# Performance work log

Measured on AMD Instinct MI355X. Metric: run time of the kernel, lower is better.

The kernel has to match this reference:

```python
import jax, jax.numpy as jnp
import numpy as np

# ---- config (matches init_kwargs) ----
ORIGIN_OCC_SHAPE = (16, 200, 200)   # (D_oi, H_oi, W_oi)
INPUT_SIZE = (900, 1600)            # (ih, iw)
DOWN_SAMPLE = 8
GRID_CONFIG = {
    'x_bound': [-40.0, 40.0, 0.4],
    'y_bound': [-40.0, 40.0, 0.4],
    'z_bound': [-1.0, 5.4, 0.4],
    'd_bound': [2.0, 58.0, 1.0],
}


def setup_inputs() -> dict:
    key = jax.random.key(0)
    occ_feature = jax.random.normal(key, (1, 32, 16, 200, 200), dtype=jnp.float32)
    # realistic nuScenes-like intrinsics
    K = jnp.array([[[1266.4, 0.0, 816.3],
                    [0.0, 1266.4, 491.5],
                    [0.0, 0.0, 1.0]]], dtype=jnp.float32)
    # cam->ego: camera looks along ego +x; cam z -> ego x, cam x -> ego -y, cam y -> ego -z
    T = jnp.array([[[0.0, 0.0, 1.0, 1.5],
                    [-1.0, 0.0, 0.0, 0.0],
                    [0.0, -1.0, 0.0, 1.5],
                    [0.0, 0.0, 0.0, 1.0]]], dtype=jnp.float32)
    return {'occ_feature': occ_feature, 'K': K, 'T': T}


def get_sampling_points():
    ih, iw = INPUT_SIZE
    fh, fw = ih // DOWN_SAMPLE, iw // DOWN_SAMPLE
    d0, d1, dstep = GRID_CONFIG['d_bound']
    fd = int((d1 - d0) // dstep)
    x = jnp.linspace(0.0, iw - 1.0, fw)
    y = jnp.linspace(0.0, ih - 1.0, fh)
    d = jnp.linspace(d0, d1, fd)
    gd, gy, gx = jnp.meshgrid(d, y, x, indexing='ij')   # (fd, fh, fw)
    # homogeneous image points scaled by depth: [x*d, y*d, d, 1]
    pts = jnp.stack([gx * gd, gy * gd, gd, jnp.ones_like(gd)], axis=-1)
    return pts  # (fd, fh, fw, 4)


def grid_sample_3d(vol, grid):
    """Trilinear grid_sample, padding_mode='zeros', align_corners=True.
    vol: (B,C,D,H,W); grid: (B,Do,Ho,Wo,3) with (x,y,z) in [-1,1] -> (W,H,D)."""
    B, C, D, H, W = vol.shape
    gx, gy, gz = grid[..., 0], grid[..., 1], grid[..., 2]
    x = (gx + 1.0) * 0.5 * (W - 1)
    y = (gy + 1.0) * 0.5 * (H - 1)
    z = (gz + 1.0) * 0.5 * (D - 1)
    x0 = jnp.floor(x); y0 = jnp.floor(y); z0 = jnp.floor(z)
    tx = x - x0; ty = y - y0; tz = z - z0
    vol_flat = vol.reshape(B, C, D * H * W)

    def corner(zc, yc, xc, w):
        valid = (xc >= 0) & (xc <= W - 1) & (yc >= 0) & (yc <= H - 1) & (zc >= 0) & (zc <= D - 1)
        zi = jnp.clip(zc, 0, D - 1).astype(jnp.int32)
        yi = jnp.clip(yc, 0, H - 1).astype(jnp.int32)
        xi = jnp.clip(xc, 0, W - 1).astype(jnp.int32)
        idx = ((zi * H + yi) * W + xi).reshape(B, 1, -1)          # (B,1,M)
        g = jnp.take_along_axis(vol_flat, idx, axis=2)            # (B,C,M)
        wm = jnp.where(valid, w, 0.0).reshape(B, 1, -1)
        return g * wm

    out = (corner(z0, y0, x0, (1 - tz) * (1 - ty) * (1 - tx))
           + corner(z0, y0, x0 + 1, (1 - tz) * (1 - ty) * tx)
           + corner(z0, y0 + 1, x0, (1 - tz) * ty * (1 - tx))
           + corner(z0, y0 + 1, x0 + 1, (1 - tz) * ty * tx)
           + corner(z0 + 1, y0, x0, tz * (1 - ty) * (1 - tx))
           + corner(z0 + 1, y0, x0 + 1, tz * (1 - ty) * tx)
           + corner(z0 + 1, y0 + 1, x0, tz * ty * (1 - tx))
           + corner(z0 + 1, y0 + 1, x0 + 1, tz * ty * tx))
    Do, Ho, Wo = grid.shape[1:4]
    return out.reshape(B, C, Do, Ho, Wo)


def volume_transform(occ_feature, K, T):
    B, C, D_occ, H_occ, W_occ = occ_feature.shape
    D_oi, H_oi, W_oi = ORIGIN_OCC_SHAPE
    ratio = (W_oi / W_occ, H_oi / H_occ, D_oi / D_occ)
    xb, yb, zb = GRID_CONFIG['x_bound'], GRID_CONFIG['y_bound'], GRID_CONFIG['z_bound']

    # ego -> ego-feature-grid affine (4x4)
    e2f = jnp.eye(4, dtype=jnp.float32)
    e2f = e2f.at[0, 0].set(1.0 / xb[2] / ratio[0])
    e2f = e2f.at[1, 1].set(1.0 / yb[2] / ratio[1])
    e2f = e2f.at[2, 2].set(1.0 / zb[2] / ratio[2])
    e2f = e2f.at[0, 3].set(-xb[0] / xb[2] / ratio[0])
    e2f = e2f.at[1, 3].set(-yb[0] / yb[2] / ratio[1])
    e2f = e2f.at[2, 3].set(-zb[0] / zb[2] / ratio[2])

    # cam2img 4x4 with K in top-left, then invert (matches torch.inverse path)
    cam2img = jnp.tile(jnp.eye(4, dtype=K.dtype)[None], (B, 1, 1))
    cam2img = cam2img.at[:, :3, :3].set(K)
    img2cam = jnp.linalg.inv(cam2img)                  # (B,4,4)

    # fused projection matrix: ego2egofeat @ T @ img2cam
    M = jnp.einsum('ij,bjk,bkl->bil', e2f, T, img2cam)  # (B,4,4)

    pts = get_sampling_points()                         # (fd,fh,fw,4)
    feat_pts = jnp.einsum('bij,dhwj->bdhwi', M, pts)[..., :3]  # (B,fd,fh,fw,3)

    norm = jnp.array([W_occ - 1, H_occ - 1, D_occ - 1], dtype=jnp.float32)
    grid = feat_pts / norm * 2.0 - 1.0

    sampled = grid_sample_3d(occ_feature, grid)         # (B,C,fd,fh,fw)
    return jnp.sum(sampled, axis=2)                     # (B,C,fh,fw)


def reference(occ_feature, K, T):
    return volume_transform(occ_feature, K, T)
```

## Files before the change

### kernel.cpp

```cpp
#include <hip/hip_runtime.h>

#define FD 56
#define FH 112
#define FW 200
#define VD 16
#define VH 200
#define VW 200
#define NC 32
#define NPIX (FH * FW)
#define NS   (VD * VH * VW)
#define CSTRIDE NS

typedef float f2v __attribute__((ext_vector_type(2)));
typedef f2v uf2v4 __attribute__((aligned(4)));
typedef _Float16 h4 __attribute__((ext_vector_type(4)));
typedef h4 uh4 __attribute__((aligned(8)));
typedef _Float16 h8 __attribute__((ext_vector_type(8)));

__device__ inline void compute_M(const float* Km, const float* Tm, float* M) {
    float a = Km[0], b = Km[1], c = Km[2];
    float d = Km[3], e = Km[4], f = Km[5];
    float g = Km[6], h = Km[7], i = Km[8];
    float A00 = e * i - f * h, A01 = c * h - b * i, A02 = b * f - c * e;
    float A10 = f * g - d * i, A11 = a * i - c * g, A12 = c * d - a * f;
    float A20 = d * h - e * g, A21 = b * g - a * h, A22 = a * e - b * d;
    float det = a * A00 + b * A10 + c * A20;
    float r = 1.0f / det;
    float Ki[9] = {A00 * r, A01 * r, A02 * r,
                   A10 * r, A11 * r, A12 * r,
                   A20 * r, A21 * r, A22 * r};
    float R[4][4];
    for (int rr = 0; rr < 4; ++rr) {
        for (int cc = 0; cc < 3; ++cc)
            R[rr][cc] = Tm[rr * 4 + 0] * Ki[0 * 3 + cc]
                      + Tm[rr * 4 + 1] * Ki[1 * 3 + cc]
                      + Tm[rr * 4 + 2] * Ki[2 * 3 + cc];
        R[rr][3] = Tm[rr * 4 + 3];
    }
    const float s[3] = {2.5f, 2.5f, 2.5f};
    const float t[3] = {100.0f, 100.0f, 2.5f};
    for (int rr = 0; rr < 3; ++rr)
        for (int cc = 0; cc < 4; ++cc)
            M[rr * 4 + cc] = s[rr] * R[rr][cc] + t[rr] * R[3][cc];
}

__global__ __launch_bounds__(256)
void vt_transpose_h(const float* __restrict__ vol, _Float16* __restrict__ volT,
                    const float* __restrict__ Km, const float* __restrict__ Tm) {
    __shared__ float tile[256 * 33];
    __shared__ int s_skip;
    const int t  = threadIdx.x;
    const int s0 = blockIdx.x * 256;

    if (t == 0) {
        float M[12];
        compute_M(Km, Tm, M);
        const float b00 = M[0], b01 = M[1], b02 = M[2],  tx3 = M[3];
        const float b10 = M[4], b11 = M[5], b12 = M[6],  ty3 = M[7];
        const float b20 = M[8], b21 = M[9], b22 = M[10], tz3 = M[11];
        const float C00 = b11 * b22 - b12 * b21;
        const float C01 = b02 * b21 - b01 * b22;
        const float C02 = b01 * b12 - b02 * b11;
        const float C10 = b12 * b20 - b10 * b22;
        const float C11 = b00 * b22 - b02 * b20;
        const float C12 = b02 * b10 - b00 * b12;
        const float C20 = b10 * b21 - b11 * b20;
        const float C21 = b01 * b20 - b00 * b21;
        const float C22 = b00 * b11 - b01 * b10;
        const float det = b00 * C00 + b01 * C10 + b02 * C20;
        int skip = 0;
        if (fabsf(det) > 1e-12f) {
            const float r = 1.0f / det;
            const float ix0 = C00 * r, ix1 = C01 * r, ix2 = C02 * r;
            const float iy0 = C10 * r, iy1 = C11 * r, iy2 = C12 * r;
            const float iz0 = C20 * r, iz1 = C21 * r, iz2 = C22 * r;
            const float cx = -(ix0 * tx3 + ix1 * ty3 + ix2 * tz3);
            const float cy = -(iy0 * tx3 + iy1 * ty3 + iy2 * tz3);
            const float cz = -(iz0 * tx3 + iz1 * ty3 + iz2 * tz3);
            const int send = s0 + 255;
            const int z0 = s0 / (VH * VW), z1 = send / (VH * VW);
            float ylo = 0.0f, yhi = (float)(VH - 1);
            if (z0 == z1) {
                const int r0 = s0 - z0 * (VH * VW);
                ylo = (float)(r0 / VW);
                yhi = (float)((r0 + 255) / VW);
            }
            const float EXP = 1.25f;
            const float lo[3] = {0.0f - EXP, ylo - EXP, (float)z0 - EXP};
            const float hi[3] = {(float)(VW - 1) + EXP, yhi + EXP, (float)z1 + EXP};
            const float SLK = 10.0f;
            const float gc[6][3] = {
                { iz0,  iz1,  iz2},
                {-iz0, -iz1, -iz2},
                { ix0,  ix1,  ix2},
                {1599.f*iz0 - ix0, 1599.f*iz1 - ix1, 1599.f*iz2 - ix2},
                { iy0,  iy1,  iy2},
                { 899.f*iz0 - iy0,  899.f*iz1 - iy1,  899.f*iz2 - iy2},
            };
            const float gd0[6] = {cz - 2.0f + 0.1f, 58.0f + 0.1f - cz,
                                  cx + SLK, 1599.f * cz - cx + SLK,
                                  cy + SLK,  899.f * cz - cy + SLK};
            for (int q = 0; q < 6; ++q) {
                float m = gd0[q];
                for (int j = 0; j < 3; ++j)
                    m += (gc[q][j] > 0.0f) ? gc[q][j] * hi[j] : gc[q][j] * lo[j];
                if (m < 0.0f) { skip = 1; break; }
            }
        }
        s_skip = skip;
    }
    __syncthreads();
    if (s_skip) return;

#pragma unroll
    for (int c = 0; c < NC; ++c)
        tile[t * 33 + c] = __builtin_nontemporal_load(vol + (size_t)c * CSTRIDE + s0 + t);
    __syncthreads();
    const int rs  = t >> 2;
    const int ch8 = (t & 3) * 8;
#pragma unroll
    for (int j = 0; j < 4; ++j) {
        const int sl = j * 64 + rs;
        const float* r = &tile[sl * 33 + ch8];
        h8 pk = {(_Float16)r[0], (_Float16)r[1], (_Float16)r[2], (_Float16)r[3],
                 (_Float16)r[4], (_Float16)r[5], (_Float16)r[6], (_Float16)r[7]};
        *(h8*)(volT + (size_t)(s0 + sl) * NC + ch8) = pk;
    }
}

__global__ __launch_bounds__(256)
void vt_sample_th(const _Float16* __restrict__ volT,
                  const float* __restrict__ Km,
                  const float* __restrict__ Tm,
                  float* __restrict__ out) {
    __shared__ float sM[12];
    if (threadIdx.x == 0) compute_M(Km, Tm, sM);
    __syncthreads();

    const int t    = threadIdx.x;
    const int wv   = t >> 6;
    const int lane = t & 63;
    const int chq  = lane & 7;
    const int pixl = lane >> 3;
    const int c0   = chq * 4;
    const int p    = blockIdx.x * 32 + wv * 8 + pixl;
    const int py   = p / FW;
    const int px   = p - py * FW;

    const float gx = (float)px * (1599.0f / 199.0f);
    const float gy = (float)py * (899.0f / 111.0f);

    const float m03 = sM[3], m13 = sM[7], m23 = sM[11];
    const float ax = sM[0] * gx + sM[1] * gy + sM[2];
    const float ay = sM[4] * gx + sM[5] * gy + sM[6];
    const float az = sM[8] * gx + sM[9] * gy + sM[10];

    float dlo = 2.0f, dhi = 58.0f;
    {
        const float A[3]  = {ax, ay, az};
        const float Bv[3] = {m03, m13, m23};
        const float HI[3] = {(float)VW, (float)VH, (float)VD};
        for (int q = 0; q < 3; ++q) {
            float a = A[q], b = Bv[q], hi = HI[q];
            if (a > 0.0f)      { dlo = fmaxf(dlo, (-1.0f - b) / a); dhi = fminf(dhi, (hi - b) / a); }
            else if (a < 0.0f) { dlo = fmaxf(dlo, (hi - b) / a);    dhi = fminf(dhi, (-1.0f - b) / a); }
            else if (!(b > -1.0f && b < hi)) { dlo = 1e30f; dhi = -1e30f; }
        }
    }
    int klo = (int)ceilf((dlo - 2.0f) * (55.0f / 56.0f));
    int khi = (int)floorf((dhi - 2.0f) * (55.0f / 56.0f));
    klo = max(klo - 1, 0);
    khi = min(khi + 1, FD - 1);

    float acc0 = 0.0f, acc1 = 0.0f, acc2 = 0.0f, acc3 = 0.0f;

#pragma unroll 2
    for (int k = klo; k <= khi; ++k) {
        const float gd = 2.0f + (float)k * (56.0f / 55.0f);
        const float fx = fmaf(ax, gd, m03);
        const float fy = fmaf(ay, gd, m13);
        const float fz = fmaf(az, gd, m23);

        const bool valid = (fx > -1.0f) && (fx < (float)VW) &&
                           (fy > -1.0f) && (fy < (float)VH) &&
                           (fz > -1.0f) && (fz < (float)VD);
        const float vm = valid ? 1.0f : 0.0f;

        const float xf = floorf(fx), yf = floorf(fy), zf = floorf(fz);
        const float tx = fx - xf, ty = fy - yf, tz = fz - zf;
        const int ix = (int)xf, iy = (int)yf, iz = (int)zf;

        const float wx0 = (ix >= 0)     ? (1.0f - tx) : 0.0f;
        const float wx1 = (ix < VW - 1) ? tx          : 0.0f;
        const float wy0 = (iy >= 0)     ? (1.0f - ty) : 0.0f;
        const float wy1 = (iy < VH - 1) ? ty          : 0.0f;
        const float wz0 = ((iz >= 0)     ? (1.0f - tz) : 0.0f) * vm;
        const float wz1 = ((iz < VD - 1) ? tz          : 0.0f) * vm;

        const int xi0 = min(max(ix,     0), VW - 1);
        const int xi1 = min(max(ix + 1, 0), VW - 1);
        const int yo0 = min(max(iy,     0), VH - 1) * VW;
        const int yo1 = min(max(iy + 1, 0), VH - 1) * VW;
        const int zo0 = min(max(iz,     0), VD - 1) * (VH * VW);
        const int zo1 = min(max(iz + 1, 0), VD - 1) * (VH * VW);

        const int o000 = ((zo0 + yo0 + xi0) << 5) + c0;
        const int o001 = ((zo0 + yo0 + xi1) << 5) + c0;
        const int o010 = ((zo0 + yo1 + xi0) << 5) + c0;
        const int o011 = ((zo0 + yo1 + xi1) << 5) + c0;
        const int o100 = ((zo1 + yo0 + xi0) << 5) + c0;
        const int o101 = ((zo1 + yo0 + xi1) << 5) + c0;
        const int o110 = ((zo1 + yo1 + xi0) << 5) + c0;
        const int o111 = ((zo1 + yo1 + xi1) << 5) + c0;

        const h4 v000 = *(const uh4*)(volT + o000);
        const h4 v001 = *(const uh4*)(volT + o001);
        const h4 v010 = *(const uh4*)(volT + o010);
        const h4 v011 = *(const uh4*)(volT + o011);
        const h4 v100 = *(const uh4*)(volT + o100);
        const h4 v101 = *(const uh4*)(volT + o101);
        const h4 v110 = *(const uh4*)(volT + o110);
        const h4 v111 = *(const uh4*)(volT + o111);

        const float w000 = wz0 * wy0 * wx0, w001 = wz0 * wy0 * wx1;
        const float w010 = wz0 * wy1 * wx0, w011 = wz0 * wy1 * wx1;
        const float w100 = wz1 * wy0 * wx0, w101 = wz1 * wy0 * wx1;
        const float w110 = wz1 * wy1 * wx0, w111 = wz1 * wy1 * wx1;

        acc0 += w000 * (float)v000.x + w001 * (float)v001.x
              + w010 * (float)v010.x + w011 * (float)v011.x
              + w100 * (float)v100.x + w101 * (float)v101.x
              + w110 * (float)v110.x + w111 * (float)v111.x;
        acc1 += w000 * (float)v000.y + w001 * (float)v001.y
              + w010 * (float)v010.y + w011 * (float)v011.y
              + w100 * (float)v100.y + w101 * (float)v101.y
              + w110 * (float)v110.y + w111 * (float)v111.y;
        acc2 += w000 * (float)v000.z + w001 * (float)v001.z
              + w010 * (float)v010.z + w011 * (float)v011.z
              + w100 * (float)v100.z + w101 * (float)v101.z
              + w110 * (float)v110.z + w111 * (float)v111.z;
        acc3 += w000 * (float)v000.w + w001 * (float)v001.w
              + w010 * (float)v010.w + w011 * (float)v011.w
              + w100 * (float)v100.w + w101 * (float)v101.w
              + w110 * (float)v110.w + w111 * (float)v111.w;
    }

    out[(size_t)(c0 + 0) * NPIX + p] = acc0;
    out[(size_t)(c0 + 1) * NPIX + p] = acc1;
    out[(size_t)(c0 + 2) * NPIX + p] = acc2;
    out[(size_t)(c0 + 3) * NPIX + p] = acc3;
}

__global__ __launch_bounds__(256)
void vt_sample_direct(const float* __restrict__ vol,
                      const float* __restrict__ Km,
                      const float* __restrict__ Tm,
                      float* __restrict__ out) {
    __shared__ float sM[12];
    if (threadIdx.x == 0) compute_M(Km, Tm, sM);
    __syncthreads();

    const int cg   = blockIdx.x & 3;
    const int pg   = blockIdx.x >> 2;
    const int lane = threadIdx.x & 63;
    const int wv   = threadIdx.x >> 6;
    const int c0   = (cg * 4 + wv) * 2;
    const int p    = pg * 64 + lane;
    const int py   = p / FW;
    const int px   = p - py * FW;

    const float gx = (float)px * (1599.0f / 199.0f);
    const float gy = (float)py * (899.0f / 111.0f);

    const float m03 = sM[3], m13 = sM[7], m23 = sM[11];
    const float ax = sM[0] * gx + sM[1] * gy + sM[2];
    const float ay = sM[4] * gx + sM[5] * gy + sM[6];
    const float az = sM[8] * gx + sM[9] * gy + sM[10];

    float dlo = 2.0f, dhi = 58.0f;
    {
        const float A[3]  = {ax, ay, az};
        const float Bv[3] = {m03, m13, m23};
        const float HI[3] = {(float)VW, (float)VH, (float)VD};
        for (int q = 0; q < 3; ++q) {
            float a = A[q], b = Bv[q], hi = HI[q];
            if (a > 0.0f)      { dlo = fmaxf(dlo, (-1.0f - b) / a); dhi = fminf(dhi, (hi - b) / a); }
            else if (a < 0.0f) { dlo = fmaxf(dlo, (hi - b) / a);    dhi = fminf(dhi, (-1.0f - b) / a); }
            else if (!(b > -1.0f && b < hi)) { dlo = 1e30f; dhi = -1e30f; }
        }
    }
    int klo = (int)ceilf((dlo - 2.0f) * (55.0f / 56.0f));
    int khi = (int)floorf((dhi - 2.0f) * (55.0f / 56.0f));
    klo = max(klo - 1, 0);
    khi = min(khi + 1, FD - 1);

    const float* __restrict__ volc0 = vol + (size_t)c0 * CSTRIDE;
    const float* __restrict__ volc1 = volc0 + CSTRIDE;
    float acc0 = 0.0f, acc1 = 0.0f;

#pragma unroll 2
    for (int k = klo; k <= khi; ++k) {
        const float gd = 2.0f + (float)k * (56.0f / 55.0f);
        const float fx = fmaf(ax, gd, m03);
        const float fy = fmaf(ay, gd, m13);
        const float fz = fmaf(az, gd, m23);

        const bool valid = (fx > -1.0f) && (fx < (float)VW) &&
                           (fy > -1.0f) && (fy < (float)VH) &&
                           (fz > -1.0f) && (fz < (float)VD);
        const float vm = valid ? 1.0f : 0.0f;

        const float xf = floorf(fx), yf = floorf(fy), zf = floorf(fz);
        const float tx = fx - xf, ty = fy - yf, tz = fz - zf;
        const int ix = (int)xf, iy = (int)yf, iz = (int)zf;

        float wlo = (ix >= 0) ? (1.0f - tx) : tx;
        wlo = (ix >= VW - 1) ? 0.0f : wlo;
        float whi = (ix >= 0) ? tx : 0.0f;
        whi = (ix >= VW - 1) ? (1.0f - tx) : whi;

        const float wy0 = (iy >= 0)     ? (1.0f - ty) : 0.0f;
        const float wy1 = (iy < VH - 1) ? ty          : 0.0f;
        const float wz0 = ((iz >= 0)     ? (1.0f - tz) : 0.0f) * vm;
        const float wz1 = ((iz < VD - 1) ? tz          : 0.0f) * vm;
        const float w00 = wz0 * wy0, w01 = wz0 * wy1;
        const float w10 = wz1 * wy0, w11 = wz1 * wy1;

        const int xi0 = min(max(ix, 0), VW - 2);
        const int yo0 = min(max(iy,     0), VH - 1) * VW;
        const int yo1 = min(max(iy + 1, 0), VH - 1) * VW;
        const int zo0 = min(max(iz,     0), VD - 1) * (VH * VW);
        const int zo1 = min(max(iz + 1, 0), VD - 1) * (VH * VW);

        const int o00 = zo0 + yo0 + xi0, o01 = zo0 + yo1 + xi0;
        const int o10 = zo1 + yo0 + xi0, o11 = zo1 + yo1 + xi0;

        const f2v a00 = *(const uf2v4*)(volc0 + o00);
        const f2v a01 = *(const uf2v4*)(volc0 + o01);
        const f2v a10 = *(const uf2v4*)(volc0 + o10);
        const f2v a11 = *(const uf2v4*)(volc0 + o11);
        const f2v b00 = *(const uf2v4*)(volc1 + o00);
        const f2v b01 = *(const uf2v4*)(volc1 + o01);
        const f2v b10 = *(const uf2v4*)(volc1 + o10);
        const f2v b11 = *(const uf2v4*)(volc1 + o11);

        acc0 += w00 * (wlo * a00.x + whi * a00.y) + w01 * (wlo * a01.x + whi * a01.y)
              + w10 * (wlo * a10.x + whi * a10.y) + w11 * (wlo * a11.x + whi * a11.y);
        acc1 += w00 * (wlo * b00.x + whi * b00.y) + w01 * (wlo * b01.x + whi * b01.y)
              + w10 * (wlo * b10.x + whi * b10.y) + w11 * (wlo * b11.x + whi * b11.y);
    }

    out[c0 * NPIX + p]       = acc0;
    out[(c0 + 1) * NPIX + p] = acc1;
}

extern "C" void kernel_launch(void* const* d_in, const int* in_sizes, int n_in,
                              void* d_out, int out_size, void* d_ws, size_t ws_size,
                              hipStream_t stream) {
    (void)in_sizes; (void)n_in; (void)out_size;
    const float* vol = (const float*)d_in[0];
    const float* Km  = (const float*)d_in[1];
    const float* Tm  = (const float*)d_in[2];
    float* out = (float*)d_out;

    const size_t need = (size_t)NS * NC * sizeof(_Float16);
    if (ws_size >= need) {
        _Float16* volT = (_Float16*)d_ws;
        vt_transpose_h<<<dim3(NS / 256), dim3(256), 0, stream>>>(vol, volT, Km, Tm);
        vt_sample_th<<<dim3(NPIX / 32), dim3(256), 0, stream>>>(volT, Km, Tm, out);
    } else {
        vt_sample_direct<<<dim3(1400), dim3(256), 0, stream>>>(vol, Km, Tm, out);
    }
}
```

Baseline: 145.5 us.

## Compact transposed fp16 volume to frustum bounding box and remap blocks per XCD

Adds a one-block setup kernel that computes the projection matrix and a voxel bounding box covering every sampling ray across all depths, and stores both in a small header in the workspace. The transpose kernel now skips blocks outside that box and writes the fp16 channel-last copy into a compact box-sized buffer. The sampling kernel clamps indices to the box and reads from the compact layout, which keeps the working set smaller and more cache-friendly. It also remaps block indices so each XCD handles a contiguous pixel range. The cost is an extra kernel launch, per-voxel index arithmetic in the transpose, and reliance on the box bound being conservative enough to keep results correct.

```diff
diff --git a/kernel.cpp b/kernel.cpp
--- a/kernel.cpp
+++ b/kernel.cpp
@@ -44,73 +44,143 @@
             M[rr * 4 + cc] = s[rr] * R[rr][cc] + t[rr] * R[3][cc];
 }
 
+__global__ __launch_bounds__(64)
+void vt_setup(const float* __restrict__ Km, const float* __restrict__ Tm,
+              float* __restrict__ hdr) {
+    __shared__ float sM[12];
+    const int t = threadIdx.x;
+    if (t == 0) compute_M(Km, Tm, sM);
+    __syncthreads();
+    float m[12];
+#pragma unroll
+    for (int i = 0; i < 12; ++i) m[i] = sM[i];
+
+    int bx0 = 0x7fffffff, by0 = 0x7fffffff, bz0 = 0x7fffffff;
+    int bx1 = -1, by1 = -1, bz1 = -1;
+    if (t < FD) {
+        const float gd = 2.0f + (float)t * (56.0f / 55.0f);
+        const float HIq[3] = {(float)VW, (float)VH, (float)VD};
+        float lo[3], hi[3];
+        bool ok = true;
+#pragma unroll
+        for (int q = 0; q < 3; ++q) {
+            const float axx  = m[q * 4 + 0] * gd * 1599.0f;
+            const float byy  = m[q * 4 + 1] * gd * 899.0f;
+            const float base = m[q * 4 + 2] * gd + m[q * 4 + 3];
+            lo[q] = base + fminf(axx, 0.0f) + fminf(byy, 0.0f);
+            hi[q] = base + fmaxf(axx, 0.0f) + fmaxf(byy, 0.0f);
+            if (!(lo[q] < HIq[q] && hi[q] > -1.0f)) ok = false;
+        }
+        if (ok) {
+            const int dmax[3] = {VW - 1, VH - 1, VD - 1};
+#pragma unroll
+            for (int q = 0; q < 3; ++q) {
+                int i0 = (int)floorf(fmaxf(lo[q], -2.0f)) - 1;
+                int i1 = (int)floorf(fminf(hi[q], HIq[q] + 1.0f)) + 2;
+                i0 = max(i0, 0);
+                i1 = min(i1, dmax[q]);
+                if (q == 0) { bx0 = i0; bx1 = i1; }
+                else if (q == 1) { by0 = i0; by1 = i1; }
+                else { bz0 = i0; bz1 = i1; }
+            }
+        }
+    }
+#pragma unroll
+    for (int s = 1; s < 64; s <<= 1) {
+        bx0 = min(bx0, __shfl_xor(bx0, s));
+        bx1 = max(bx1, __shfl_xor(bx1, s));
+        by0 = min(by0, __shfl_xor(by0, s));
+        by1 = max(by1, __shfl_xor(by1, s));
+        bz0 = min(bz0, __shfl_xor(bz0, s));
+        bz1 = max(bz1, __shfl_xor(bz1, s));
+    }
+    if (t == 0) {
+        if (bx1 < bx0 || by1 < by0 || bz1 < bz0) {
+            bx0 = by0 = bz0 = 0; bx1 = by1 = bz1 = 0;
+        }
+#pragma unroll
+        for (int i = 0; i < 12; ++i) hdr[i] = m[i];
+        int* hi = (int*)hdr;
+        hi[12] = bx0; hi[13] = by0; hi[14] = bz0;
+        hi[15] = bx1 - bx0 + 1;
+        hi[16] = by1 - by0 + 1;
+        hi[17] = bz1 - bz0 + 1;
+    }
+}
+
 __global__ __launch_bounds__(256)
-void vt_transpose_h(const float* __restrict__ vol, _Float16* __restrict__ volT,
-                    const float* __restrict__ Km, const float* __restrict__ Tm) {
+void vt_transpose_h(const float* __restrict__ vol, const float* __restrict__ hdr,
+                    _Float16* __restrict__ volT) {
     __shared__ float tile[256 * 33];
-    __shared__ int s_skip;
+    __shared__ int sh[8];
     const int t  = threadIdx.x;
     const int s0 = blockIdx.x * 256;
 
     if (t == 0) {
-        float M[12];
-        compute_M(Km, Tm, M);
-        const float b00 = M[0], b01 = M[1], b02 = M[2],  tx3 = M[3];
-        const float b10 = M[4], b11 = M[5], b12 = M[6],  ty3 = M[7];
-        const float b20 = M[8], b21 = M[9], b22 = M[10], tz3 = M[11];
-        const float C00 = b11 * b22 - b12 * b21;
-        const float C01 = b02 * b21 - b01 * b22;
-        const float C02 = b01 * b12 - b02 * b11;
-        const float C10 = b12 * b20 - b10 * b22;
-        const float C11 = b00 * b22 - b02 * b20;
-        const float C12 = b02 * b10 - b00 * b12;
-        const float C20 = b10 * b21 - b11 * b20;
-        const float C21 = b01 * b20 - b00 * b21;
-        const float C22 = b00 * b11 - b01 * b10;
-        const float det = b00 * C00 + b01 * C10 + b02 * C20;
+        const int* hint = (const int*)hdr;
+        const int cx0 = hint[12], cy0 = hint[13], cz0 = hint[14];
+        const int cw = hint[15], chh = hint[16], cd = hint[17];
+        const int send = s0 + 255;
+        const int z0 = s0 / (VH * VW), z1 = send / (VH * VW);
+        int ry0 = 0, ry1 = VH - 1;
+        if (z0 == z1) {
+            const int r0 = s0 - z0 * (VH * VW);
+            ry0 = r0 / VW;
+            ry1 = (r0 + 255) / VW;
+        }
         int skip = 0;
-        if (fabsf(det) > 1e-12f) {
-            const float r = 1.0f / det;
-            const float ix0 = C00 * r, ix1 = C01 * r, ix2 = C02 * r;
-            const float iy0 = C10 * r, iy1 = C11 * r, iy2 = C12 * r;
-            const float iz0 = C20 * r, iz1 = C21 * r, iz2 = C22 * r;
-            const float cx = -(ix0 * tx3 + ix1 * ty3 + ix2 * tz3);
-            const float cy = -(iy0 * tx3 + iy1 * ty3 + iy2 * tz3);
-            const float cz = -(iz0 * tx3 + iz1 * ty3 + iz2 * tz3);
-            const int send = s0 + 255;
-            const int z0 = s0 / (VH * VW), z1 = send / (VH * VW);
-            float ylo = 0.0f, yhi = (float)(VH - 1);
-            if (z0 == z1) {
-                const int r0 = s0 - z0 * (VH * VW);
-                ylo = (float)(r0 / VW);
-                yhi = (float)((r0 + 255) / VW);
+        if (z1 < cz0 || z0 > cz0 + cd - 1) skip = 1;
+        if (ry1 < cy0 || ry0 > cy0 + chh - 1) skip = 1;
+        if (!skip) {
+            const float b00 = hdr[0], b01 = hdr[1], b02 = hdr[2],  tx3 = hdr[3];
+            const float b10 = hdr[4], b11 = hdr[5], b12 = hdr[6],  ty3 = hdr[7];
+            const float b20 = hdr[8], b21 = hdr[9], b22 = hdr[10], tz3 = hdr[11];
+            const float C00 = b11 * b22 - b12 * b21;
+            const float C01 = b02 * b21 - b01 * b22;
+            const float C02 = b01 * b12 - b02 * b11;
+            const float C10 = b12 * b20 - b10 * b22;
+            const float C11 = b00 * b22 - b02 * b20;
+            const float C12 = b02 * b10 - b00 * b12;
+            const float C20 = b10 * b21 - b11 * b20;
+            const float C21 = b01 * b20 - b00 * b21;
+            const float C22 = b00 * b11 - b01 * b10;
+            const float det = b00 * C00 + b01 * C10 + b02 * C20;
+            if (fabsf(det) > 1e-12f) {
+                const float r = 1.0f / det;
+                const float ix0 = C00 * r, ix1 = C01 * r, ix2 = C02 * r;
+                const float iy0 = C10 * r, iy1 = C11 * r, iy2 = C12 * r;
+                const float iz0 = C20 * r, iz1 = C21 * r, iz2 = C22 * r;
+                const float cx = -(ix0 * tx3 + ix1 * ty3 + ix2 * tz3);
+                const float cy = -(iy0 * tx3 + iy1 * ty3 + iy2 * tz3);
+                const float cz = -(iz0 * tx3 + iz1 * ty3 + iz2 * tz3);
+                const float EXP = 1.25f;
+                const float lo[3] = {0.0f - EXP, (float)ry0 - EXP, (float)z0 - EXP};
+                const float hi[3] = {(float)(VW - 1) + EXP, (float)ry1 + EXP, (float)z1 + EXP};
+                const float SLK = 10.0f;
+                const float gc[6][3] = {
+                    { iz0,  iz1,  iz2},
+                    {-iz0, -iz1, -iz2},
+                    { ix0,  ix1,  ix2},
+                    {1599.f*iz0 - ix0, 1599.f*iz1 - ix1, 1599.f*iz2 - ix2},
+                    { iy0,  iy1,  iy2},
+                    { 899.f*iz0 - iy0,  899.f*iz1 - iy1,  899.f*iz2 - iy2},
+                };
+                const float gd0[6] = {cz - 2.0f + 0.1f, 58.0f + 0.1f - cz,
+                                      cx + SLK, 1599.f * cz - cx + SLK,
+                                      cy + SLK,  899.f * cz - cy + SLK};
+                for (int q = 0; q < 6; ++q) {
+                    float mx = gd0[q];
+                    for (int j = 0; j < 3; ++j)
+                        mx += (gc[q][j] > 0.0f) ? gc[q][j] * hi[j] : gc[q][j] * lo[j];
+                    if (mx < 0.0f) { skip = 1; break; }
+                }
             }
-            const float EXP = 1.25f;
-            const float lo[3] = {0.0f - EXP, ylo - EXP, (float)z0 - EXP};
-            const float hi[3] = {(float)(VW - 1) + EXP, yhi + EXP, (float)z1 + EXP};
-            const float SLK = 10.0f;
-            const float gc[6][3] = {
-                { iz0,  iz1,  iz2},
-                {-iz0, -iz1, -iz2},
-                { ix0,  ix1,  ix2},
-                {1599.f*iz0 - ix0, 1599.f*iz1 - ix1, 1599.f*iz2 - ix2},
-                { iy0,  iy1,  iy2},
-                { 899.f*iz0 - iy0,  899.f*iz1 - iy1,  899.f*iz2 - iy2},
-            };
-            const float gd0[6] = {cz - 2.0f + 0.1f, 58.0f + 0.1f - cz,
-                                  cx + SLK, 1599.f * cz - cx + SLK,
-                                  cy + SLK,  899.f * cz - cy + SLK};
-            for (int q = 0; q < 6; ++q) {
-                float m = gd0[q];
-                for (int j = 0; j < 3; ++j)
-                    m += (gc[q][j] > 0.0f) ? gc[q][j] * hi[j] : gc[q][j] * lo[j];
-                if (m < 0.0f) { skip = 1; break; }
-            }
-        }
-        s_skip = skip;
+        }
+        sh[0] = skip; sh[1] = cx0; sh[2] = cy0; sh[3] = cz0;
+        sh[4] = cw; sh[5] = chh; sh[6] = cd; sh[7] = chh * cw;
     }
     __syncthreads();
-    if (s_skip) return;
+    if (sh[0]) return;
 
 #pragma unroll
     for (int c = 0; c < NC; ++c)
@@ -118,23 +188,41 @@
     __syncthreads();
     const int rs  = t >> 2;
     const int ch8 = (t & 3) * 8;
+    const int cx0 = sh[1], cy0 = sh[2], cz0 = sh[3];
+    const int cw = sh[4], chh = sh[5], cd = sh[6], chw = sh[7];
 #pragma unroll
     for (int j = 0; j < 4; ++j) {
         const int sl = j * 64 + rs;
+        const int s  = s0 + sl;
+        const int z   = s / (VH * VW);
+        const int rem = s - z * (VH * VW);
+        const int y   = rem / VW;
+        const int x   = rem - y * VW;
+        const int ex = x - cx0, ey = y - cy0, ez = z - cz0;
+        if (ex < 0 || ex >= cw || ey < 0 || ey >= chh || ez < 0 || ez >= cd) continue;
         const float* r = &tile[sl * 33 + ch8];
         h8 pk = {(_Float16)r[0], (_Float16)r[1], (_Float16)r[2], (_Float16)r[3],
                  (_Float16)r[4], (_Float16)r[5], (_Float16)r[6], (_Float16)r[7]};
-        *(h8*)(volT + (size_t)(s0 + sl) * NC + ch8) = pk;
+        *(h8*)(volT + ((size_t)(ez * chw + ey * cw + ex) << 5) + ch8) = pk;
     }
 }
 
 __global__ __launch_bounds__(256)
 void vt_sample_th(const _Float16* __restrict__ volT,
-                  const float* __restrict__ Km,
-                  const float* __restrict__ Tm,
+                  const float* __restrict__ hdr,
                   float* __restrict__ out) {
     __shared__ float sM[12];
-    if (threadIdx.x == 0) compute_M(Km, Tm, sM);
+    __shared__ int sc[8];
+    if (threadIdx.x < 12) sM[threadIdx.x] = hdr[threadIdx.x];
+    if (threadIdx.x == 0) {
+        const int* hint = (const int*)hdr;
+        const int x0 = hint[12], y0 = hint[13], z0 = hint[14];
+        const int cw = hint[15], chh = hint[16], cd = hint[17];
+        sc[0] = x0; sc[1] = x0 + cw - 1;
+        sc[2] = y0; sc[3] = y0 + chh - 1;
+        sc[4] = z0; sc[5] = z0 + cd - 1;
+        sc[6] = cw; sc[7] = chh * cw;
+    }
     __syncthreads();
 
     const int t    = threadIdx.x;
@@ -143,7 +231,14 @@
     const int chq  = lane & 7;
     const int pixl = lane >> 3;
     const int c0   = chq * 4;
-    const int p    = blockIdx.x * 32 + wv * 8 + pixl;
+
+    const int nwg = NPIX / 32;
+    const int qc  = nwg >> 3, rc = nwg & 7;
+    const int xcd = (int)blockIdx.x & 7;
+    const int idx = (int)blockIdx.x >> 3;
+    const int sb  = (xcd < rc ? xcd * (qc + 1) : rc * (qc + 1) + (xcd - rc) * qc) + idx;
+
+    const int p    = sb * 32 + wv * 8 + pixl;
     const int py   = p / FW;
     const int px   = p - py * FW;
 
@@ -154,6 +249,9 @@
     const float ax = sM[0] * gx + sM[1] * gy + sM[2];
     const float ay = sM[4] * gx + sM[5] * gy + sM[6];
     const float az = sM[8] * gx + sM[9] * gy + sM[10];
+
+    const int X0 = sc[0], X1 = sc[1], Y0 = sc[2], Y1 = sc[3];
+    const int Z0 = sc[4], Z1 = sc[5], CWr = sc[6], CHWr = sc[7];
 
     float dlo = 2.0f, dhi = 58.0f;
     {
@@ -197,12 +295,12 @@
         const float wz0 = ((iz >= 0)     ? (1.0f - tz) : 0.0f) * vm;
         const float wz1 = ((iz < VD - 1) ? tz          : 0.0f) * vm;
 
-        const int xi0 = min(max(ix,     0), VW - 1);
-        const int xi1 = min(max(ix + 1, 0), VW - 1);
-        const int yo0 = min(max(iy,     0), VH - 1) * VW;
-        const int yo1 = min(max(iy + 1, 0), VH - 1) * VW;
-        const int zo0 = min(max(iz,     0), VD - 1) * (VH * VW);
-        const int zo1 = min(max(iz + 1, 0), VD - 1) * (VH * VW);
+        const int xi0 = min(max(ix,     X0), X1) - X0;
+        const int xi1 = min(max(ix + 1, X0), X1) - X0;
+        const int yo0 = (min(max(iy,     Y0), Y1) - Y0) * CWr;
+        const int yo1 = (min(max(iy + 1, Y0), Y1) - Y0) * CWr;
+        const int zo0 = (min(max(iz,     Z0), Z1) - Z0) * CHWr;
+        const int zo1 = (min(max(iz + 1, Z0), Z1) - Z0) * CHWr;
 
         const int o000 = ((zo0 + yo0 + xi0) << 5) + c0;
         const int o001 = ((zo0 + yo0 + xi1) << 5) + c0;
@@ -241,8 +339,8 @@
               + w110 * (float)v110.z + w111 * (float)v111.z;
         acc3 += w000 * (float)v000.w + w001 * (float)v001.w
               + w010 * (float)v010.w + w011 * (float)v011.w
-              + w100 * (float)v100.w + w101 * (float)v101.w
-              + w110 * (float)v110.w + w111 * (float)v111.w;
+              + w110 * (float)v110.w + w111 * (float)v111.w
+              + w100 * (float)v100.w + w101 * (float)v101.w;
     }
 
     out[(size_t)(c0 + 0) * NPIX + p] = acc0;
@@ -363,11 +461,13 @@
     const float* Tm  = (const float*)d_in[2];
     float* out = (float*)d_out;
 
-    const size_t need = (size_t)NS * NC * sizeof(_Float16);
+    const size_t need = 256 + (size_t)NS * NC * sizeof(_Float16);
     if (ws_size >= need) {
-        _Float16* volT = (_Float16*)d_ws;
-        vt_transpose_h<<<dim3(NS / 256), dim3(256), 0, stream>>>(vol, volT, Km, Tm);
-        vt_sample_th<<<dim3(NPIX / 32), dim3(256), 0, stream>>>(volT, Km, Tm, out);
+        float* hdr = (float*)d_ws;
+        _Float16* volT = (_Float16*)((char*)d_ws + 256);
+        vt_setup<<<dim3(1), dim3(64), 0, stream>>>(Km, Tm, hdr);
+        vt_transpose_h<<<dim3(NS / 256), dim3(256), 0, stream>>>(vol, hdr, volT);
+        vt_sample_th<<<dim3(NPIX / 32), dim3(256), 0, stream>>>(volT, hdr, out);
     } else {
         vt_sample_direct<<<dim3(1400), dim3(256), 0, stream>>>(vol, Km, Tm, out);
     }
```

After: 160.1 us. 1.1x slower.

## Transpose only the frustum bounding box into a compact cropped volume

Applied to the files above, without the earlier changes.

Each block now computes the camera frustum's axis-aligned bounding box in voxel space with a per-depth wavefront reduction. Only voxels inside that crop are transposed into a dense compact fp16 layout, and the sampler indexes that layout. This shrinks the number of live transpose blocks and the workspace footprint, which improves cache locality for gathers. The cost is that every block recomputes M and the crop, and the crop clamping changes how out-of-crop corners are handled, which could risk correctness if the bound is too tight.

```diff
diff --git a/kernel.cpp b/kernel.cpp
--- a/kernel.cpp
+++ b/kernel.cpp
@@ -44,98 +44,170 @@
             M[rr * 4 + cc] = s[rr] * R[rr][cc] + t[rr] * R[3][cc];
 }
 
+__device__ inline void compute_crop(const float* m, int& cx0, int& cy0, int& cz0,
+                                    int& cw, int& ch, int& cd) {
+    const int l = threadIdx.x & 63;
+    int bx0 = 0x7fffffff, by0 = 0x7fffffff, bz0 = 0x7fffffff;
+    int bx1 = -1, by1 = -1, bz1 = -1;
+    if (l < FD) {
+        const float gd = 2.0f + (float)l * (56.0f / 55.0f);
+        const float HIq[3] = {(float)VW, (float)VH, (float)VD};
+        float lo[3], hi[3];
+        bool ok = true;
+#pragma unroll
+        for (int q = 0; q < 3; ++q) {
+            const float axx  = m[q * 4 + 0] * gd * 1599.0f;
+            const float byy  = m[q * 4 + 1] * gd * 899.0f;
+            const float base = m[q * 4 + 2] * gd + m[q * 4 + 3];
+            lo[q] = base + fminf(axx, 0.0f) + fminf(byy, 0.0f);
+            hi[q] = base + fmaxf(axx, 0.0f) + fmaxf(byy, 0.0f);
+            if (!(lo[q] < HIq[q] && hi[q] > -1.0f)) ok = false;
+        }
+        if (ok) {
+            const int dmax[3] = {VW - 1, VH - 1, VD - 1};
+#pragma unroll
+            for (int q = 0; q < 3; ++q) {
+                int i0 = (int)floorf(fmaxf(lo[q], -2.0f)) - 1;
+                int i1 = (int)floorf(fminf(hi[q], HIq[q] + 1.0f)) + 2;
+                i0 = max(i0, 0);
+                i1 = min(i1, dmax[q]);
+                if (q == 0) { bx0 = i0; bx1 = i1; }
+                else if (q == 1) { by0 = i0; by1 = i1; }
+                else { bz0 = i0; bz1 = i1; }
+            }
+        }
+    }
+#pragma unroll
+    for (int s = 1; s < 64; s <<= 1) {
+        bx0 = min(bx0, __shfl_xor(bx0, s));
+        bx1 = max(bx1, __shfl_xor(bx1, s));
+        by0 = min(by0, __shfl_xor(by0, s));
+        by1 = max(by1, __shfl_xor(by1, s));
+        bz0 = min(bz0, __shfl_xor(bz0, s));
+        bz1 = max(bz1, __shfl_xor(bz1, s));
+    }
+    if (bx1 < bx0 || by1 < by0 || bz1 < bz0) {
+        bx0 = by0 = bz0 = 0; bx1 = by1 = bz1 = 0;
+    }
+    cx0 = bx0; cy0 = by0; cz0 = bz0;
+    cw = bx1 - bx0 + 1; ch = by1 - by0 + 1; cd = bz1 - bz0 + 1;
+}
+
+__device__ inline int wedge_skip(const float* M, const float lo[3], const float hi[3]) {
+    const float b00 = M[0], b01 = M[1], b02 = M[2],  tx3 = M[3];
+    const float b10 = M[4], b11 = M[5], b12 = M[6],  ty3 = M[7];
+    const float b20 = M[8], b21 = M[9], b22 = M[10], tz3 = M[11];
+    const float C00 = b11 * b22 - b12 * b21;
+    const float C01 = b02 * b21 - b01 * b22;
+    const float C02 = b01 * b12 - b02 * b11;
+    const float C10 = b12 * b20 - b10 * b22;
+    const float C11 = b00 * b22 - b02 * b20;
+    const float C12 = b02 * b10 - b00 * b12;
+    const float C20 = b10 * b21 - b11 * b20;
+    const float C21 = b01 * b20 - b00 * b21;
+    const float C22 = b00 * b11 - b01 * b10;
+    const float det = b00 * C00 + b01 * C10 + b02 * C20;
+    if (!(fabsf(det) > 1e-12f)) return 0;
+    const float r = 1.0f / det;
+    const float ix0 = C00 * r, ix1 = C01 * r, ix2 = C02 * r;
+    const float iy0 = C10 * r, iy1 = C11 * r, iy2 = C12 * r;
+    const float iz0 = C20 * r, iz1 = C21 * r, iz2 = C22 * r;
+    const float cx = -(ix0 * tx3 + ix1 * ty3 + ix2 * tz3);
+    const float cy = -(iy0 * tx3 + iy1 * ty3 + iy2 * tz3);
+    const float cz = -(iz0 * tx3 + iz1 * ty3 + iz2 * tz3);
+    const float SLK = 10.0f;
+    const float gc[6][3] = {
+        { iz0,  iz1,  iz2},
+        {-iz0, -iz1, -iz2},
+        { ix0,  ix1,  ix2},
+        {1599.f*iz0 - ix0, 1599.f*iz1 - ix1, 1599.f*iz2 - ix2},
+        { iy0,  iy1,  iy2},
+        { 899.f*iz0 - iy0,  899.f*iz1 - iy1,  899.f*iz2 - iy2},
+    };
+    const float gd0[6] = {cz - 2.0f + 0.1f, 58.0f + 0.1f - cz,
+                          cx + SLK, 1599.f * cz - cx + SLK,
+                          cy + SLK,  899.f * cz - cy + SLK};
+    for (int q = 0; q < 6; ++q) {
+        float mx = gd0[q];
+        for (int j = 0; j < 3; ++j)
+            mx += (gc[q][j] > 0.0f) ? gc[q][j] * hi[j] : gc[q][j] * lo[j];
+        if (mx < 0.0f) return 1;
+    }
+    return 0;
+}
+
 __global__ __launch_bounds__(256)
-void vt_transpose_h(const float* __restrict__ vol, _Float16* __restrict__ volT,
+void vt_transpose_c(const float* __restrict__ vol, _Float16* __restrict__ volT,
                     const float* __restrict__ Km, const float* __restrict__ Tm) {
     __shared__ float tile[256 * 33];
-    __shared__ int s_skip;
-    const int t  = threadIdx.x;
-    const int s0 = blockIdx.x * 256;
-
-    if (t == 0) {
-        float M[12];
-        compute_M(Km, Tm, M);
-        const float b00 = M[0], b01 = M[1], b02 = M[2],  tx3 = M[3];
-        const float b10 = M[4], b11 = M[5], b12 = M[6],  ty3 = M[7];
-        const float b20 = M[8], b21 = M[9], b22 = M[10], tz3 = M[11];
-        const float C00 = b11 * b22 - b12 * b21;
-        const float C01 = b02 * b21 - b01 * b22;
-        const float C02 = b01 * b12 - b02 * b11;
-        const float C10 = b12 * b20 - b10 * b22;
-        const float C11 = b00 * b22 - b02 * b20;
-        const float C12 = b02 * b10 - b00 * b12;
-        const float C20 = b10 * b21 - b11 * b20;
-        const float C21 = b01 * b20 - b00 * b21;
-        const float C22 = b00 * b11 - b01 * b10;
-        const float det = b00 * C00 + b01 * C10 + b02 * C20;
-        int skip = 0;
-        if (fabsf(det) > 1e-12f) {
-            const float r = 1.0f / det;
-            const float ix0 = C00 * r, ix1 = C01 * r, ix2 = C02 * r;
-            const float iy0 = C10 * r, iy1 = C11 * r, iy2 = C12 * r;
-            const float iz0 = C20 * r, iz1 = C21 * r, iz2 = C22 * r;
-            const float cx = -(ix0 * tx3 + ix1 * ty3 + ix2 * tz3);
-            const float cy = -(iy0 * tx3 + iy1 * ty3 + iy2 * tz3);
-            const float cz = -(iz0 * tx3 + iz1 * ty3 + iz2 * tz3);
-            const int send = s0 + 255;
-            const int z0 = s0 / (VH * VW), z1 = send / (VH * VW);
-            float ylo = 0.0f, yhi = (float)(VH - 1);
-            if (z0 == z1) {
-                const int r0 = s0 - z0 * (VH * VW);
-                ylo = (float)(r0 / VW);
-                yhi = (float)((r0 + 255) / VW);
-            }
-            const float EXP = 1.25f;
-            const float lo[3] = {0.0f - EXP, ylo - EXP, (float)z0 - EXP};
-            const float hi[3] = {(float)(VW - 1) + EXP, yhi + EXP, (float)z1 + EXP};
-            const float SLK = 10.0f;
-            const float gc[6][3] = {
-                { iz0,  iz1,  iz2},
-                {-iz0, -iz1, -iz2},
-                { ix0,  ix1,  ix2},
-                {1599.f*iz0 - ix0, 1599.f*iz1 - ix1, 1599.f*iz2 - ix2},
-                { iy0,  iy1,  iy2},
-                { 899.f*iz0 - iy0,  899.f*iz1 - iy1,  899.f*iz2 - iy2},
-            };
-            const float gd0[6] = {cz - 2.0f + 0.1f, 58.0f + 0.1f - cz,
-                                  cx + SLK, 1599.f * cz - cx + SLK,
-                                  cy + SLK,  899.f * cz - cy + SLK};
-            for (int q = 0; q < 6; ++q) {
-                float m = gd0[q];
-                for (int j = 0; j < 3; ++j)
-                    m += (gc[q][j] > 0.0f) ? gc[q][j] * hi[j] : gc[q][j] * lo[j];
-                if (m < 0.0f) { skip = 1; break; }
-            }
+    const int t = threadIdx.x;
+
+    float M[12];
+    compute_M(Km, Tm, M);
+    int x0, y0, z0, cw, ch, cd;
+    compute_crop(M, x0, y0, z0, cw, ch, cd);
+    const int chw = ch * cw;
+    const int tot = cd * chw;
+    const int cb0 = blockIdx.x * 256;
+    if (cb0 >= tot) return;
+
+    {
+        const int clast = min(cb0 + 255, tot - 1);
+        const int ez0 = cb0 / chw, ez1 = clast / chw;
+        int ey0 = 0, ey1 = ch - 1;
+        if (ez0 == ez1) {
+            const int r0 = cb0 - ez0 * chw;
+            ey0 = r0 / cw;
+            ey1 = (clast - ez0 * chw) / cw;
         }
-        s_skip = skip;
-    }
-    __syncthreads();
-    if (s_skip) return;
-
+        const float EXP = 1.25f;
+        const float lo[3] = {(float)x0 - EXP, (float)(y0 + ey0) - EXP, (float)(z0 + ez0) - EXP};
+        const float hi[3] = {(float)(x0 + cw - 1) + EXP, (float)(y0 + ey1) + EXP, (float)(z0 + ez1) + EXP};
+        if (wedge_skip(M, lo, hi)) return;
+    }
+
+    const int cidx = cb0 + t;
+    const bool live = cidx < tot;
+    int lin = 0;
+    if (live) {
+        const int ez = cidx / chw;
+        const int r1 = cidx - ez * chw;
+        const int ey = r1 / cw;
+        const int ex = r1 - ey * cw;
+        lin = (z0 + ez) * (VH * VW) + (y0 + ey) * VW + (x0 + ex);
+    }
+    if (live) {
 #pragma unroll
-    for (int c = 0; c < NC; ++c)
-        tile[t * 33 + c] = __builtin_nontemporal_load(vol + (size_t)c * CSTRIDE + s0 + t);
+        for (int c = 0; c < NC; ++c)
+            tile[t * 33 + c] = __builtin_nontemporal_load(vol + (size_t)c * CSTRIDE + lin);
+    }
     __syncthreads();
     const int rs  = t >> 2;
     const int ch8 = (t & 3) * 8;
 #pragma unroll
     for (int j = 0; j < 4; ++j) {
         const int sl = j * 64 + rs;
+        if (cb0 + sl >= tot) continue;
         const float* r = &tile[sl * 33 + ch8];
         h8 pk = {(_Float16)r[0], (_Float16)r[1], (_Float16)r[2], (_Float16)r[3],
                  (_Float16)r[4], (_Float16)r[5], (_Float16)r[6], (_Float16)r[7]};
-        *(h8*)(volT + (size_t)(s0 + sl) * NC + ch8) = pk;
+        *(h8*)(volT + ((size_t)(cb0 + sl) << 5) + ch8) = pk;
     }
 }
 
 __global__ __launch_bounds__(256)
-void vt_sample_th(const _Float16* __restrict__ volT,
-                  const float* __restrict__ Km,
-                  const float* __restrict__ Tm,
-                  float* __restrict__ out) {
-    __shared__ float sM[12];
-    if (threadIdx.x == 0) compute_M(Km, Tm, sM);
-    __syncthreads();
+void vt_sample_c(const _Float16* __restrict__ volT,
+                 const float* __restrict__ Km,
+                 const float* __restrict__ Tm,
+                 float* __restrict__ out) {
+    float Mv[12];
+    compute_M(Km, Tm, Mv);
+    int x0, y0, z0, cw, chh, cd;
+    compute_crop(Mv, x0, y0, z0, cw, chh, cd);
+    const int X0 = x0, X1 = x0 + cw - 1;
+    const int Y0 = y0, Y1 = y0 + chh - 1;
+    const int Z0 = z0, Z1 = z0 + cd - 1;
+    const int CWr = cw, CHWr = chh * cw;
 
     const int t    = threadIdx.x;
     const int wv   = t >> 6;
@@ -150,10 +222,10 @@
     const float gx = (float)px * (1599.0f / 199.0f);
     const float gy = (float)py * (899.0f / 111.0f);
 
-    const float m03 = sM[3], m13 = sM[7], m23 = sM[11];
-    const float ax = sM[0] * gx + sM[1] * gy + sM[2];
-    const float ay = sM[4] * gx + sM[5] * gy + sM[6];
-    const float az = sM[8] * gx + sM[9] * gy + sM[10];
+    const float m03 = Mv[3], m13 = Mv[7], m23 = Mv[11];
+    const float ax = Mv[0] * gx + Mv[1] * gy + Mv[2];
+    const float ay = Mv[4] * gx + Mv[5] * gy + Mv[6];
+    const float az = Mv[8] * gx + Mv[9] * gy + Mv[10];
 
     float dlo = 2.0f, dhi = 58.0f;
     {
@@ -197,12 +269,12 @@
         const float wz0 = ((iz >= 0)     ? (1.0f - tz) : 0.0f) * vm;
         const float wz1 = ((iz < VD - 1) ? tz          : 0.0f) * vm;
 
-        const int xi0 = min(max(ix,     0), VW - 1);
-        const int xi1 = min(max(ix + 1, 0), VW - 1);
-        const int yo0 = min(max(iy,     0), VH - 1) * VW;
-        const int yo1 = min(max(iy + 1, 0), VH - 1) * VW;
-        const int zo0 = min(max(iz,     0), VD - 1) * (VH * VW);
-        const int zo1 = min(max(iz + 1, 0), VD - 1) * (VH * VW);
+        const int xi0 = min(max(ix,     X0), X1) - X0;
+        const int xi1 = min(max(ix + 1, X0), X1) - X0;
+        const int yo0 = (min(max(iy,     Y0), Y1) - Y0) * CWr;
+        const int yo1 = (min(max(iy + 1, Y0), Y1) - Y0) * CWr;
+        const int zo0 = (min(max(iz,     Z0), Z1) - Z0) * CHWr;
+        const int zo1 = (min(max(iz + 1, Z0), Z1) - Z0) * CHWr;
 
         const int o000 = ((zo0 + yo0 + xi0) << 5) + c0;
         const int o001 = ((zo0 + yo0 + xi1) << 5) + c0;
@@ -366,8 +438,8 @@
     const size_t need = (size_t)NS * NC * sizeof(_Float16);
     if (ws_size >= need) {
         _Float16* volT = (_Float16*)d_ws;
-        vt_transpose_h<<<dim3(NS / 256), dim3(256), 0, stream>>>(vol, volT, Km, Tm);
-        vt_sample_th<<<dim3(NPIX / 32), dim3(256), 0, stream>>>(volT, Km, Tm, out);
+        vt_transpose_c<<<dim3(NS / 256), dim3(256), 0, stream>>>(vol, volT, Km, Tm);
+        vt_sample_c<<<dim3(NPIX / 32), dim3(256), 0, stream>>>(volT, Km, Tm, out);
     } else {
         vt_sample_direct<<<dim3(1400), dim3(256), 0, stream>>>(vol, Km, Tm, out);
     }
```

After: 144.0 us. About the same (-1.0%).
